# Optimization experiments

Measured on AMD Instinct MI355X. Metric: run time of the kernel, lower is better.

## Reference

```python
import jax, jax.numpy as jnp
import numpy as np

N_NODES = 100000
N_EDGES = 1600000
NFEATS, NHIDS, NOUT = 128, 128, 64


def _gcn_conv(x, W, b, src, dst, n_nodes):
    # PyG GCNConv: linear transform, then symmetric-normalized aggregation
    # over A + I (self-loops added), then bias.
    h = x @ W                                        # [N, out]
    loop = jnp.arange(n_nodes, dtype=src.dtype)
    s = jnp.concatenate([src, loop])                 # [E + N]
    d = jnp.concatenate([dst, loop])                 # [E + N]
    deg = jax.ops.segment_sum(jnp.ones_like(d, dtype=h.dtype), d,
                              num_segments=n_nodes)  # degree of A + I
    dinv = jnp.where(deg > 0, jax.lax.rsqrt(deg), 0.0)
    norm = dinv[s] * dinv[d]                         # [E + N]
    msg = h[s] * norm[:, None]                       # gather + scale
    out = jax.ops.segment_sum(msg, d, num_segments=n_nodes)  # scatter-add
    return out + b


def setup_inputs() -> dict:
    key = jax.random.key(0)
    k1, k2, k3, k4 = jax.random.split(key, 4)
    edge_index = jax.random.randint(k1, (2, N_EDGES), 0, N_NODES, dtype=jnp.int64)
    x = jax.random.normal(k2, (N_NODES, NFEATS), dtype=jnp.float32)
    W1 = jax.random.normal(k3, (NFEATS, NHIDS), dtype=jnp.float32) / np.sqrt(NFEATS)
    b1 = jnp.zeros((NHIDS,), dtype=jnp.float32)
    W2 = jax.random.normal(k4, (NHIDS, NOUT), dtype=jnp.float32) / np.sqrt(NHIDS)
    b2 = jnp.zeros((NOUT,), dtype=jnp.float32)
    return {"edge_index": edge_index, "x": x, "W1": W1, "b1": b1,
            "W2": W2, "b2": b2}


def reference(edge_index, x, W1, b1, W2, b2):
    src, dst = edge_index[0], edge_index[1]
    n = x.shape[0]
    h = jax.nn.relu(_gcn_conv(x, W1, b1, src, dst, n))
    # dropout(p=0.5, train=False) is the identity in eval mode
    out = _gcn_conv(h, W2, b2, src, dst, n)
    return out
```

## Files before the change

### kernel.cpp

```cpp
#include <hip/hip_runtime.h>
#include <cstdint>
#include <cstddef>

#define NFEATS 128
#define NHIDS  128
#define NOUT   64
#define SB     256
#define CHUNK  4096

using bf16x8 = __attribute__((ext_vector_type(8))) short;
using f32x4  = __attribute__((ext_vector_type(4))) float;
using u32x4  = __attribute__((ext_vector_type(4))) unsigned int;

__device__ inline unsigned short f2bf(float f) {
    union { float f; unsigned int u; } v; v.f = f;
    unsigned int r = (v.u + 0x7FFFu + ((v.u >> 16) & 1u)) >> 16;
    return (unsigned short)r;
}
__device__ inline float bflo(unsigned int u) { return __uint_as_float(u << 16); }
__device__ inline float bfhi(unsigned int u) { return __uint_as_float(u & 0xFFFF0000u); }

__global__ void detect_kernel(const void* p, int* flag, long long n_nodes) {
    const long long* q = (const long long*)p;
    long long v = q[threadIdx.x];
    int bad = (v < 0 || v >= n_nodes) ? 1 : 0;
    unsigned long long m = __ballot(bad);
    if (threadIdx.x == 0) *flag = (m != 0ULL) ? 1 : 0;
}

__global__ void hist_kernel(const void* __restrict__ edges, const int* __restrict__ flag,
                            int* __restrict__ histT, int ne, int nch, int nbkt) {
    __shared__ int h[1024];
    int c = blockIdx.x, t = threadIdx.x;
    for (int i = t; i < nbkt; i += 512) h[i] = 0;
    __syncthreads();
    int beg = c * CHUNK, end = min(ne, beg + CHUNK);
    bool is32 = (*flag != 0);
    for (int i = beg + t; i < end; i += 512) {
        int d = is32 ? ((const int*)edges)[ne + i]
                     : (int)((const long long*)edges)[ne + i];
        atomicAdd(&h[d >> 8], 1);
    }
    __syncthreads();
    for (int i = t; i < nbkt; i += 512)
        histT[i * nch + c] = h[i];
}

__global__ void scan_block(const int* __restrict__ v, int* __restrict__ incl,
                           int* __restrict__ partial, int n) {
    __shared__ int sh[256];
    int t = threadIdx.x;
    int i = blockIdx.x * 256 + t;
    sh[t] = (i < n) ? v[i] : 0;
    __syncthreads();
    for (int off = 1; off < 256; off <<= 1) {
        int add = (t >= off) ? sh[t - off] : 0;
        __syncthreads();
        sh[t] += add;
        __syncthreads();
    }
    if (i < n) incl[i] = sh[t];
    if (t == 255) partial[blockIdx.x] = sh[255];
}

__global__ void scan_partials(int* partial, int nb) {
    __shared__ int sh[512];
    __shared__ int carry;
    int t = threadIdx.x;
    if (t == 0) carry = 0;
    __syncthreads();
    for (int base = 0; base < nb; base += 512) {
        int idx = base + t;
        sh[t] = (idx < nb) ? partial[idx] : 0;
        __syncthreads();
        for (int off = 1; off < 512; off <<= 1) {
            int add = (t >= off) ? sh[t - off] : 0;
            __syncthreads();
            sh[t] += add;
            __syncthreads();
        }
        int excl = carry + ((t == 0) ? 0 : sh[t - 1]);
        if (idx < nb) partial[idx] = excl;
        __syncthreads();
        if (t == 0) carry += sh[511];
        __syncthreads();
    }
}

__global__ void finalize_scan(const int* __restrict__ incl, const int* __restrict__ v,
                              const int* __restrict__ partial,
                              int* __restrict__ excl, int m) {
    int i = blockIdx.x * blockDim.x + threadIdx.x;
    if (i < m) excl[i] = partial[i >> 8] + incl[i] - v[i];
}

__global__ void scatter_chunks(const void* __restrict__ edges, const int* __restrict__ flag,
                               const int* __restrict__ chunk_base,
                               unsigned int* __restrict__ ebuf,
                               int ne, int nch, int nbkt) {
    __shared__ int cur[1024];
    int c = blockIdx.x, t = threadIdx.x;
    for (int i = t; i < nbkt; i += 512) cur[i] = chunk_base[i * nch + c];
    __syncthreads();
    int beg = c * CHUNK, end = min(ne, beg + CHUNK);
    bool is32 = (*flag != 0);
    for (int i = beg + t; i < end; i += 512) {
        int s, d;
        if (is32) {
            s = ((const int*)edges)[i];
            d = ((const int*)edges)[ne + i];
        } else {
            s = (int)((const long long*)edges)[i];
            d = (int)((const long long*)edges)[ne + i];
        }
        int pos = atomicAdd(&cur[d >> 8], 1);
        ebuf[pos] = ((unsigned int)s << 8) | (unsigned int)(d & (SB - 1));
    }
}

__global__ void bucket_finalize(const unsigned int* __restrict__ ebuf,
                                const int* __restrict__ chunk_base,
                                int* __restrict__ row_ptr, float* __restrict__ dinv,
                                int* __restrict__ csr_src,
                                int n, int e, int nch, int nbkt) {
    __shared__ int deg[SB];
    __shared__ int incl[SB];
    __shared__ int cur[SB];
    int b = blockIdx.x, t = threadIdx.x;
    int node0 = b * SB;
    int nn = min(SB, n - node0);
    int base = chunk_base[b * nch];
    int bend = (b == nbkt - 1) ? e : chunk_base[(b + 1) * nch];

    deg[t] = 0;
    __syncthreads();
    for (int i = base + t; i < bend; i += SB)
        atomicAdd(&deg[ebuf[i] & (SB - 1)], 1);
    __syncthreads();

    incl[t] = deg[t];
    __syncthreads();
    for (int off = 1; off < SB; off <<= 1) {
        int add = (t >= off) ? incl[t - off] : 0;
        __syncthreads();
        incl[t] += add;
        __syncthreads();
    }
    int lrow = base + incl[t] - deg[t];
    cur[t] = lrow;
    if (t < nn) {
        row_ptr[node0 + t] = lrow;
        dinv[node0 + t]    = rsqrtf((float)(deg[t] + 1));
    }
    if (b == nbkt - 1 && t == 0) row_ptr[n] = e;
    __syncthreads();

    for (int i = base + t; i < bend; i += SB) {
        unsigned int r = ebuf[i];
        int pos = atomicAdd(&cur[r & (SB - 1)], 1);
        csr_src[pos] = (int)(r >> 8);
    }
}

__global__ void w_pack(const float* __restrict__ W1, unsigned short* __restrict__ Wf1,
                       const float* __restrict__ W2, unsigned short* __restrict__ Wf2) {
    int i = blockIdx.x * blockDim.x + threadIdx.x;
    if (i < 128 * 128) {
        int k = i >> 7, n = i & 127;
        Wf1[(((k >> 3) * 128) + n) * 8 + (k & 7)] = f2bf(W1[i]);
    }
    if (i < 128 * 64) {
        int k = i >> 6, n = i & 63;
        Wf2[(((k >> 3) * 64) + n) * 8 + (k & 7)] = f2bf(W2[i]);
    }
}

template <int NC, bool F32IN>
__launch_bounds__(256)
__global__ void gemm_mfma(const void* __restrict__ Xin,
                          const unsigned short* __restrict__ Wf,
                          const float* __restrict__ dinv,
                          unsigned short* __restrict__ hs, int nrows) {
    constexpr int K = 128;
    __shared__ __align__(16) unsigned short Xl[16 * 128 * 8];

    const int tid  = threadIdx.x;
    const int row0 = blockIdx.x * 128;

    for (int i = tid; i < 128 * 32; i += 256) {
        int r  = i >> 5;
        int c4 = i & 31;
        int gr = row0 + r;
        ushort4 v = make_ushort4(0, 0, 0, 0);
        if (gr < nrows) {
            if (F32IN) {
                float4 f = ((const float4*)((const float*)Xin + (size_t)gr * K))[c4];
                v.x = f2bf(f.x); v.y = f2bf(f.y); v.z = f2bf(f.z); v.w = f2bf(f.w);
            } else {
                v = ((const ushort4*)((const unsigned short*)Xin + (size_t)gr * K))[c4];
            }
        }
        int k   = c4 * 4;
        int grp = k >> 3;
        int j0  = k & 7;
        *(ushort4*)(Xl + ((size_t)grp * 128 + r) * 8 + j0) = v;
    }
    __syncthreads();

    const int wv   = tid >> 6;
    const int lane = tid & 63;
    const int m    = lane & 15;
    const int q    = lane >> 4;

    bf16x8 af[2][4];
#pragma unroll
    for (int h = 0; h < 2; ++h)
#pragma unroll
        for (int kt = 0; kt < 4; ++kt)
            af[h][kt] = *(const bf16x8*)(Xl + (((kt * 4 + q) * 128) + h * 64 + wv * 16 + m) * 8);

    int   rbase[2];
    float dv[2][4];
#pragma unroll
    for (int h = 0; h < 2; ++h) {
        rbase[h] = row0 + h * 64 + wv * 16 + q * 4;
#pragma unroll
        for (int i = 0; i < 4; ++i)
            dv[h][i] = (rbase[h] + i < nrows) ? dinv[rbase[h] + i] : 0.f;
    }

#pragma unroll
    for (int nt = 0; nt < NC / 16; ++nt) {
        bf16x8 bfr[4];
#pragma unroll
        for (int kt = 0; kt < 4; ++kt)
            bfr[kt] = *(const bf16x8*)(Wf + (((size_t)(kt * 4 + q) * NC) + nt * 16 + m) * 8);
#pragma unroll
        for (int h = 0; h < 2; ++h) {
            f32x4 acc = {0.f, 0.f, 0.f, 0.f};
#pragma unroll
            for (int kt = 0; kt < 4; ++kt)
                acc = __builtin_amdgcn_mfma_f32_16x16x32_bf16(af[h][kt], bfr[kt], acc, 0, 0, 0);
#pragma unroll
            for (int i = 0; i < 4; ++i) {
                int g = rbase[h] + i;
                if (g < nrows)
                    hs[(size_t)g * NC + nt * 16 + m] = f2bf(acc[i] * dv[h][i]);
            }
        }
    }
}

template <int F, bool RELU, bool OUTBF>
__launch_bounds__(256)
__global__ void aggregate_bf16(const int* __restrict__ row_ptr,
                               const int* __restrict__ csr_src,
                               const uint4* __restrict__ hsu,
                               const float* __restrict__ dinv,
                               const float* __restrict__ b,
                               void* __restrict__ out, int n) {
    constexpr int TPN  = F / 8;
    constexpr int NPB  = 256 / TPN;
    constexpr int CH   = 16;
    constexpr int NCSR = CH / TPN;
    int node = blockIdx.x * NPB + threadIdx.x / TPN;
    int t    = threadIdx.x % TPN;
    if (node >= n) return;
    const int lane = threadIdx.x & 63;
    const int gb   = lane & ~(TPN - 1);

    uint4 u = hsu[(size_t)node * TPN + t];
    float a[8];
    a[0] = bflo(u.x); a[1] = bfhi(u.x); a[2] = bflo(u.y); a[3] = bfhi(u.y);
    a[4] = bflo(u.z); a[5] = bfhi(u.z); a[6] = bflo(u.w); a[7] = bfhi(u.w);

    int beg = row_ptr[node], end = row_ptr[node + 1];

    if (beg < end) {
        const u32x4* hb = (const u32x4*)hsu;
        u32x4 v[CH];
        int sva, svb;
        int base = beg;

        {
            const int* pc0 = csr_src + min(base + t, end - 1);
            asm volatile("global_load_dword %0, %1, off" : "=&v"(sva) : "v"(pc0));
            if (NCSR == 2) {
                const int* pc1 = csr_src + min(base + TPN + t, end - 1);
                asm volatile("global_load_dword %0, %1, off" : "=&v"(svb) : "v"(pc1));
            }
        }
        asm volatile("s_waitcnt vmcnt(0)");
        __builtin_amdgcn_sched_barrier(0);

        while (true) {
            int rem = min(CH, end - base);

#pragma unroll
            for (int j = 0; j < CH; ++j) {
                int jj = min(j, rem - 1);
                int sj;
                if (TPN == 16) {
                    sj = __shfl(sva, gb + jj, 64);
                } else {
                    int s0 = __shfl(sva, gb + (jj & 7), 64);
                    int s1 = __shfl(svb, gb + (jj & 7), 64);
                    sj = (jj < 8) ? s0 : s1;
                }
                const u32x4* p = hb + (size_t)sj * TPN + t;
                asm volatile("global_load_dwordx4 %0, %1, off" : "=&v"(v[j]) : "v"(p));
            }

            int  nbase = base + CH;
            bool more  = nbase < end;
            if (more) {
                const int* pc0 = csr_src + min(nbase + t, end - 1);
                asm volatile("global_load_dword %0, %1, off" : "=&v"(sva) : "v"(pc0));
                if (NCSR == 2) {
                    const int* pc1 = csr_src + min(nbase + TPN + t, end - 1);
                    asm volatile("global_load_dword %0, %1, off" : "=&v"(svb) : "v"(pc1));
                }
                if (NCSR == 1) asm volatile("s_waitcnt vmcnt(1)");
                else           asm volatile("s_waitcnt vmcnt(2)");
            } else {
                asm volatile("s_waitcnt vmcnt(0)");
            }
            __builtin_amdgcn_sched_barrier(0);

#pragma unroll
            for (int j = 0; j < CH; ++j) {
                if (j < rem) {
                    unsigned int x0 = v[j][0], x1 = v[j][1], x2 = v[j][2], x3 = v[j][3];
                    a[0] += bflo(x0); a[1] += bfhi(x0);
                    a[2] += bflo(x1); a[3] += bfhi(x1);
                    a[4] += bflo(x2); a[5] += bfhi(x2);
                    a[6] += bflo(x3); a[7] += bfhi(x3);
                }
            }

            if (!more) break;
            base = nbase;
            asm volatile("s_waitcnt vmcnt(0)");
            __builtin_amdgcn_sched_barrier(0);
        }
    }

    float dvn = dinv[node];
    float4 b0 = ((const float4*)b)[2 * t];
    float4 b1 = ((const float4*)b)[2 * t + 1];
    float o[8];
    o[0] = a[0] * dvn + b0.x; o[1] = a[1] * dvn + b0.y;
    o[2] = a[2] * dvn + b0.z; o[3] = a[3] * dvn + b0.w;
    o[4] = a[4] * dvn + b1.x; o[5] = a[5] * dvn + b1.y;
    o[6] = a[6] * dvn + b1.z; o[7] = a[7] * dvn + b1.w;
    if (RELU) {
#pragma unroll
        for (int j = 0; j < 8; ++j) o[j] = fmaxf(o[j], 0.f);
    }
    if (OUTBF) {
        uint4 ov;
        ov.x = (unsigned int)f2bf(o[0]) | ((unsigned int)f2bf(o[1]) << 16);
        ov.y = (unsigned int)f2bf(o[2]) | ((unsigned int)f2bf(o[3]) << 16);
        ov.z = (unsigned int)f2bf(o[4]) | ((unsigned int)f2bf(o[5]) << 16);
        ov.w = (unsigned int)f2bf(o[6]) | ((unsigned int)f2bf(o[7]) << 16);
        ((uint4*)out)[(size_t)node * TPN + t] = ov;
    } else {
        float4* op = (float4*)out + (size_t)node * (F / 4) + 2 * t;
        op[0] = make_float4(o[0], o[1], o[2], o[3]);
        op[1] = make_float4(o[4], o[5], o[6], o[7]);
    }
}

extern "C" void kernel_launch(void* const* d_in, const int* in_sizes, int n_in,
                              void* d_out, int out_size, void* d_ws, size_t ws_size,
                              hipStream_t stream) {
    const void*  edge = d_in[0];
    const float* x    = (const float*)d_in[1];
    const float* W1   = (const float*)d_in[2];
    const float* b1   = (const float*)d_in[3];
    const float* W2   = (const float*)d_in[4];
    const float* b2   = (const float*)d_in[5];
    float* out = (float*)d_out;

    const int E    = in_sizes[0] / 2;
    const int N    = in_sizes[1] / NFEATS;
    const int NBKT = (N + SB - 1) / SB;
    const int NCH  = (E + CHUNK - 1) / CHUNK;
    const int M    = NBKT * NCH;

    char* w = (char*)d_ws;
    auto carve = [&](size_t bytes) { void* p = w; w += (bytes + 255) & ~(size_t)255; return p; };
    int*            flag       = (int*)           carve(256);
    int*            histT      = (int*)           carve(sizeof(int) * (size_t)M);
    int*            incl       = (int*)           carve(sizeof(int) * (size_t)M);
    int*            partial    = (int*)           carve(sizeof(int) * 4096);
    int*            chunk_base = (int*)           carve(sizeof(int) * (size_t)M);
    int*            row_ptr    = (int*)           carve(sizeof(int) * ((size_t)N + 1));
    float*          dinv       = (float*)         carve(sizeof(float) * (size_t)N);
    unsigned int*   ebuf       = (unsigned int*)  carve(sizeof(int) * (size_t)E);
    int*            csr_src    = (int*)           carve(sizeof(int) * (size_t)E);
    unsigned short* Wf1        = (unsigned short*)carve(2 * (size_t)NFEATS * NHIDS);
    unsigned short* Wf2        = (unsigned short*)carve(2 * (size_t)NHIDS * NOUT);
    unsigned short* hs1        = (unsigned short*)carve(2 * (size_t)N * NHIDS);
    unsigned short* h1         = (unsigned short*)carve(2 * (size_t)N * NHIDS);
    unsigned short* hs2        = (unsigned short*)carve(2 * (size_t)N * NOUT);

    const int B   = 256;
    const int nbS = (M + 255) / 256;

    detect_kernel<<<1, 64, 0, stream>>>(edge, flag, (long long)N);

    hist_kernel<<<NCH, 512, 0, stream>>>(edge, flag, histT, E, NCH, NBKT);
    scan_block<<<nbS, 256, 0, stream>>>(histT, incl, partial, M);
    scan_partials<<<1, 512, 0, stream>>>(partial, nbS);
    finalize_scan<<<nbS, 256, 0, stream>>>(incl, histT, partial, chunk_base, M);
    scatter_chunks<<<NCH, 512, 0, stream>>>(edge, flag, chunk_base, ebuf, E, NCH, NBKT);
    bucket_finalize<<<NBKT, SB, 0, stream>>>(ebuf, chunk_base, row_ptr, dinv, csr_src,
                                             N, E, NCH, NBKT);

    w_pack<<<(128 * 128 + B - 1) / B, B, 0, stream>>>(W1, Wf1, W2, Wf2);

    gemm_mfma<NHIDS, true><<<(N + 127) / 128, B, 0, stream>>>(x, Wf1, dinv, hs1, N);
    {
        constexpr int NPB = 256 / (NHIDS / 8);
        aggregate_bf16<NHIDS, true, true><<<(N + NPB - 1) / NPB, B, 0, stream>>>(
            row_ptr, csr_src, (const uint4*)hs1, dinv, b1, h1, N);
    }

    gemm_mfma<NOUT, false><<<(N + 127) / 128, B, 0, stream>>>(h1, Wf2, dinv, hs2, N);
    {
        constexpr int NPB = 256 / (NOUT / 8);
        aggregate_bf16<NOUT, false, false><<<(N + NPB - 1) / NPB, B, 0, stream>>>(
            row_ptr, csr_src, (const uint4*)hs2, dinv, b2, out, N);
    }
}
```

Baseline: 279.4 us.

## Fuse layer-1 aggregation with layer-2 GEMM and locally sort edge scatter

The layer-1 aggregation kernel now also performs the ReLU, the bf16 pack and the layer-2 MFMA GEMM (scaled by dinv) in shared memory. This removes the h1 intermediate write/read and one kernel launch. Separately, scatter_chunks now counting-sorts each chunk's edges by bucket in LDS before writing them out, so global stores to ebuf are contiguous instead of scattered. In exchange it uses more LDS and barriers per block, and the fused kernel's 16-node blocks may limit occupancy.

Result: faster. 252.0 us (-9.8%).

```diff
diff --git a/kernel.cpp b/kernel.cpp
--- a/kernel.cpp
+++ b/kernel.cpp
@@ -98,24 +98,70 @@
                                const int* __restrict__ chunk_base,
                                unsigned int* __restrict__ ebuf,
                                int ne, int nch, int nbkt) {
-    __shared__ int cur[1024];
+    __shared__ int cnt[512];
+    __shared__ int cursor[512];
+    __shared__ int delta[512];
+    __shared__ unsigned int   srt[CHUNK];
+    __shared__ unsigned short bkl[CHUNK];
     int c = blockIdx.x, t = threadIdx.x;
-    for (int i = t; i < nbkt; i += 512) cur[i] = chunk_base[i * nch + c];
-    __syncthreads();
+    if (t < nbkt) cnt[t] = 0;
+    int cb = (t < nbkt) ? chunk_base[t * nch + c] : 0;
+    __syncthreads();
+
     int beg = c * CHUNK, end = min(ne, beg + CHUNK);
+    int nloc = end - beg;
     bool is32 = (*flag != 0);
-    for (int i = beg + t; i < end; i += 512) {
-        int s, d;
-        if (is32) {
-            s = ((const int*)edges)[i];
-            d = ((const int*)edges)[ne + i];
-        } else {
-            s = (int)((const long long*)edges)[i];
-            d = (int)((const long long*)edges)[ne + i];
-        }
-        int pos = atomicAdd(&cur[d >> 8], 1);
-        ebuf[pos] = ((unsigned int)s << 8) | (unsigned int)(d & (SB - 1));
-    }
+
+    unsigned int rec[8];
+    int bk[8];
+#pragma unroll
+    for (int r = 0; r < 8; ++r) {
+        int i = beg + t + r * 512;
+        bk[r] = -1;
+        if (i < end) {
+            int s, d;
+            if (is32) {
+                s = ((const int*)edges)[i];
+                d = ((const int*)edges)[ne + i];
+            } else {
+                s = (int)((const long long*)edges)[i];
+                d = (int)((const long long*)edges)[ne + i];
+            }
+            rec[r] = ((unsigned int)s << 8) | (unsigned int)(d & (SB - 1));
+            bk[r]  = d >> 8;
+            atomicAdd(&cnt[bk[r]], 1);
+        }
+    }
+    __syncthreads();
+
+    int v0 = (t < nbkt) ? cnt[t] : 0;
+    cursor[t] = v0;
+    __syncthreads();
+    for (int off = 1; off < 512; off <<= 1) {
+        int add = (t >= off) ? cursor[t - off] : 0;
+        __syncthreads();
+        cursor[t] += add;
+        __syncthreads();
+    }
+    int incl = cursor[t];
+    __syncthreads();
+    int lb = incl - v0;
+    cursor[t] = lb;
+    if (t < nbkt) delta[t] = cb - lb;
+    __syncthreads();
+
+#pragma unroll
+    for (int r = 0; r < 8; ++r) {
+        if (bk[r] >= 0) {
+            int pos = atomicAdd(&cursor[bk[r]], 1);
+            srt[pos] = rec[r];
+            bkl[pos] = (unsigned short)bk[r];
+        }
+    }
+    __syncthreads();
+
+    for (int i = t; i < nloc; i += 512)
+        ebuf[delta[bkl[i]] + i] = srt[i];
 }
 
 __global__ void bucket_finalize(const unsigned int* __restrict__ ebuf,
@@ -247,6 +293,139 @@
                 if (g < nrows)
                     hs[(size_t)g * NC + nt * 16 + m] = f2bf(acc[i] * dv[h][i]);
             }
+        }
+    }
+}
+
+__launch_bounds__(256)
+__global__ void aggregate_fused_l1(const int* __restrict__ row_ptr,
+                                   const int* __restrict__ csr_src,
+                                   const uint4* __restrict__ hsu,
+                                   const float* __restrict__ dinv,
+                                   const float* __restrict__ b,
+                                   const unsigned short* __restrict__ Wf2,
+                                   unsigned short* __restrict__ hs2, int n) {
+    constexpr int TPN = 16;
+    constexpr int NPB = 16;
+    constexpr int CH  = 16;
+
+    __shared__ __align__(16) unsigned short h1t[16 * 136];
+    __shared__ float dl[16];
+    __shared__ __align__(16) unsigned short outt[16 * 64];
+
+    const int node0 = blockIdx.x * NPB;
+    const int nl    = threadIdx.x / TPN;
+    const int t     = threadIdx.x % TPN;
+    const int node  = min(node0 + nl, n - 1);
+    const int lane  = threadIdx.x & 63;
+    const int gb    = lane & ~(TPN - 1);
+
+    uint4 u = hsu[(size_t)node * TPN + t];
+    float a[8];
+    a[0] = bflo(u.x); a[1] = bfhi(u.x); a[2] = bflo(u.y); a[3] = bfhi(u.y);
+    a[4] = bflo(u.z); a[5] = bfhi(u.z); a[6] = bflo(u.w); a[7] = bfhi(u.w);
+
+    int beg = row_ptr[node], end = row_ptr[node + 1];
+
+    if (beg < end) {
+        const u32x4* hb = (const u32x4*)hsu;
+        u32x4 v[CH];
+        int sva;
+        int base = beg;
+
+        {
+            const int* pc0 = csr_src + min(base + t, end - 1);
+            asm volatile("global_load_dword %0, %1, off" : "=&v"(sva) : "v"(pc0));
+        }
+        asm volatile("s_waitcnt vmcnt(0)");
+        __builtin_amdgcn_sched_barrier(0);
+
+        while (true) {
+            int rem = min(CH, end - base);
+
+#pragma unroll
+            for (int j = 0; j < CH; ++j) {
+                int jj = min(j, rem - 1);
+                int sj = __shfl(sva, gb + jj, 64);
+                const u32x4* p = hb + (size_t)sj * TPN + t;
+                asm volatile("global_load_dwordx4 %0, %1, off" : "=&v"(v[j]) : "v"(p));
+            }
+
+            int  nbase = base + CH;
+            bool more  = nbase < end;
+            if (more) {
+                const int* pc0 = csr_src + min(nbase + t, end - 1);
+                asm volatile("global_load_dword %0, %1, off" : "=&v"(sva) : "v"(pc0));
+                asm volatile("s_waitcnt vmcnt(1)");
+            } else {
+                asm volatile("s_waitcnt vmcnt(0)");
+            }
+            __builtin_amdgcn_sched_barrier(0);
+
+#pragma unroll
+            for (int j = 0; j < CH; ++j) {
+                if (j < rem) {
+                    unsigned int x0 = v[j][0], x1 = v[j][1], x2 = v[j][2], x3 = v[j][3];
+                    a[0] += bflo(x0); a[1] += bfhi(x0);
+                    a[2] += bflo(x1); a[3] += bfhi(x1);
+                    a[4] += bflo(x2); a[5] += bfhi(x2);
+                    a[6] += bflo(x3); a[7] += bfhi(x3);
+                }
+            }
+
+            if (!more) break;
+            base = nbase;
+            asm volatile("s_waitcnt vmcnt(0)");
+            __builtin_amdgcn_sched_barrier(0);
+        }
+    }
+
+    float dvn = dinv[node];
+    float4 b0 = ((const float4*)b)[2 * t];
+    float4 b1 = ((const float4*)b)[2 * t + 1];
+    float o[8];
+    o[0] = a[0] * dvn + b0.x; o[1] = a[1] * dvn + b0.y;
+    o[2] = a[2] * dvn + b0.z; o[3] = a[3] * dvn + b0.w;
+    o[4] = a[4] * dvn + b1.x; o[5] = a[5] * dvn + b1.y;
+    o[6] = a[6] * dvn + b1.z; o[7] = a[7] * dvn + b1.w;
+#pragma unroll
+    for (int j = 0; j < 8; ++j) o[j] = fmaxf(o[j], 0.f);
+
+    uint4 ov;
+    ov.x = (unsigned int)f2bf(o[0]) | ((unsigned int)f2bf(o[1]) << 16);
+    ov.y = (unsigned int)f2bf(o[2]) | ((unsigned int)f2bf(o[3]) << 16);
+    ov.z = (unsigned int)f2bf(o[4]) | ((unsigned int)f2bf(o[5]) << 16);
+    ov.w = (unsigned int)f2bf(o[6]) | ((unsigned int)f2bf(o[7]) << 16);
+    *(uint4*)((char*)h1t + (size_t)nl * 272 + t * 16) = ov;
+    if (t == 0) dl[nl] = dvn;
+    __syncthreads();
+
+    {
+        const int wv = threadIdx.x >> 6;
+        const int m  = lane & 15;
+        const int q  = lane >> 4;
+
+        f32x4 acc = {0.f, 0.f, 0.f, 0.f};
+#pragma unroll
+        for (int kt = 0; kt < 4; ++kt) {
+            bf16x8 af  = *(const bf16x8*)((const char*)h1t + (size_t)m * 272 + q * 16 + kt * 64);
+            bf16x8 bfr = *(const bf16x8*)(Wf2 + (((size_t)(kt * 4 + q) * 64) + wv * 16 + m) * 8);
+            acc = __builtin_amdgcn_mfma_f32_16x16x32_bf16(af, bfr, acc, 0, 0, 0);
+        }
+#pragma unroll
+        for (int i = 0; i < 4; ++i) {
+            int nd = q * 4 + i;
+            outt[nd * 64 + wv * 16 + m] = f2bf(acc[i] * dl[nd]);
+        }
+    }
+    __syncthreads();
+
+    {
+        int i = threadIdx.x;
+        if (i < 128) {
+            int gnode = node0 + (i >> 3);
+            if (gnode < n)
+                ((uint4*)hs2)[(size_t)gnode * 8 + (i & 7)] = ((const uint4*)outt)[i];
         }
     }
 }
@@ -402,7 +581,6 @@
     unsigned short* Wf1        = (unsigned short*)carve(2 * (size_t)NFEATS * NHIDS);
     unsigned short* Wf2        = (unsigned short*)carve(2 * (size_t)NHIDS * NOUT);
     unsigned short* hs1        = (unsigned short*)carve(2 * (size_t)N * NHIDS);
-    unsigned short* h1         = (unsigned short*)carve(2 * (size_t)N * NHIDS);
     unsigned short* hs2        = (unsigned short*)carve(2 * (size_t)N * NOUT);
 
     const int B   = 256;
@@ -421,13 +599,10 @@
     w_pack<<<(128 * 128 + B - 1) / B, B, 0, stream>>>(W1, Wf1, W2, Wf2);
 
     gemm_mfma<NHIDS, true><<<(N + 127) / 128, B, 0, stream>>>(x, Wf1, dinv, hs1, N);
-    {
-        constexpr int NPB = 256 / (NHIDS / 8);
-        aggregate_bf16<NHIDS, true, true><<<(N + NPB - 1) / NPB, B, 0, stream>>>(
-            row_ptr, csr_src, (const uint4*)hs1, dinv, b1, h1, N);
-    }
-
-    gemm_mfma<NOUT, false><<<(N + 127) / 128, B, 0, stream>>>(h1, Wf2, dinv, hs2, N);
+
+    aggregate_fused_l1<<<(N + 15) / 16, B, 0, stream>>>(
+        row_ptr, csr_src, (const uint4*)hs1, dinv, b1, Wf2, hs2, N);
+
     {
         constexpr int NPB = 256 / (NOUT / 8);
         aggregate_bf16<NOUT, false, false><<<(N + NPB - 1) / NPB, B, 0, stream>>>(
```
